# Performance work log

Hardware: AMD Instinct MI355X
Metric: run time of the kernel (lower is better)

The kernel has to match this reference:

```python
import jax, jax.numpy as jnp
import numpy as np

D_MODEL = 1024
MAX_LEN = 2048
BATCH = 4


def _causal_mask(max_len):
    # tril ones -> 0 on/below diag, -inf above (added to scores BEFORE scaling,
    # matching the original module's order of operations)
    return jnp.where(jnp.tril(jnp.ones((max_len, max_len), dtype=bool)), 0.0, -jnp.inf).astype(jnp.float32)


def setup_inputs() -> dict:
    key = jax.random.key(0)
    ks = jax.random.split(key, 9)
    s = 1.0 / np.sqrt(D_MODEL)  # torch Linear default init scale (uniform bound)
    return {
        "encoded_q": jax.random.normal(ks[0], (BATCH, MAX_LEN, D_MODEL), jnp.float32),
        "encoded_k": jax.random.normal(ks[1], (BATCH, MAX_LEN, D_MODEL), jnp.float32),
        "encoded_v": jax.random.normal(ks[2], (BATCH, MAX_LEN, D_MODEL), jnp.float32),
        "W_q": jax.random.uniform(ks[3], (D_MODEL, D_MODEL), jnp.float32, -s, s),
        "b_q": jax.random.uniform(ks[4], (D_MODEL,), jnp.float32, -s, s),
        "W_k": jax.random.uniform(ks[5], (D_MODEL, D_MODEL), jnp.float32, -s, s),
        "b_k": jax.random.uniform(ks[6], (D_MODEL,), jnp.float32, -s, s),
        "W_v": jax.random.uniform(ks[7], (D_MODEL, D_MODEL), jnp.float32, -s, s),
        "b_v": jax.random.uniform(ks[8], (D_MODEL,), jnp.float32, -s, s),
        "parameter_mask": 1,
    }


def reference(encoded_q, encoded_k, encoded_v, W_q, b_q, W_k, b_k, W_v, b_v, parameter_mask):
    # torch Linear: y = x @ W.T + b
    q = jnp.einsum("bsd,ed->bse", encoded_q, W_q) + b_q  # [B,S,D]
    k = jnp.einsum("bsd,ed->bse", encoded_k, W_k) + b_k
    v = jnp.einsum("bsd,ed->bse", encoded_v, W_v) + b_v
    values = jnp.einsum("bqd,bkd->bqk", q, k)  # [B,S,S]
    if parameter_mask:
        values = values + _causal_mask(values.shape[-1])
    scaled = values / jnp.sqrt(jnp.float32(D_MODEL))
    attn = jax.nn.softmax(scaled, axis=-1)
    return jnp.einsum("bqk,bkd->bqd", attn, v)  # [B,S,D]
```

## Files before the change

### kernel.cpp

```cpp
#include <hip/hip_runtime.h>

typedef __bf16 bf16;
typedef __attribute__((ext_vector_type(8))) __bf16 bf16x8;
typedef __attribute__((ext_vector_type(4))) __bf16 bf16x4;
typedef __attribute__((ext_vector_type(4))) float f32x4;

#define S_LEN 2048
#define DM 1024
#define NB 4

__device__ __forceinline__ void async_copy16(const void* g, void* l)
{
    __builtin_amdgcn_global_load_lds(
        (const __attribute__((address_space(1))) unsigned int*)g,
        (__attribute__((address_space(3))) unsigned int*)l,
        16, 0, 0);
}

#define VM_WAIT8 asm volatile("s_waitcnt vmcnt(8)" ::: "memory")
#define VM_WAIT0 asm volatile("s_waitcnt vmcnt(0)" ::: "memory")
#define LGKM0    asm volatile("s_waitcnt lgkmcnt(0)" ::: "memory")
#define BAR      asm volatile("s_barrier" ::: "memory")


__device__ __forceinline__ void stage_issue(const char* aGk, size_t aRow32,
                                            const char* bGk, size_t bRow32,
                                            char* aL, char* bL)
{
#pragma unroll
    for (int i = 0; i < 4; i++) {
        async_copy16(aGk + i * aRow32, aL + i * 4096);
        async_copy16(bGk + i * bRow32, bL + i * 4096);
    }
}

__device__ __forceinline__ void read_frags(const char* bufA, const char* bufB,
                                           int wr, int wc, int l16, int quad,
                                           bf16x8 (&af)[2][4], bf16x8 (&bfr)[2][4])
{
    const int swz = l16 & 7;
#pragma unroll
    for (int kk = 0; kk < 2; kk++) {
        const int col = (((kk << 2) + quad) ^ swz) << 4;
#pragma unroll
        for (int t = 0; t < 4; t++) {
            af[kk][t]  = *(const bf16x8*)(bufA + (wr * 64 + t * 16 + l16) * 128 + col);
            bfr[kk][t] = *(const bf16x8*)(bufB + (wc * 64 + t * 16 + l16) * 128 + col);
        }
    }
}

__device__ __forceinline__ void mfma_all(const bf16x8 (&af)[2][4],
                                         const bf16x8 (&bfr)[2][4],
                                         f32x4 (&acc)[4][4])
{
#pragma unroll
    for (int kk = 0; kk < 2; kk++)
#pragma unroll
        for (int rt = 0; rt < 4; rt++)
#pragma unroll
            for (int ct = 0; ct < 4; ct++)
                acc[rt][ct] = __builtin_amdgcn_mfma_f32_16x16x32_bf16(
                    af[kk][rt], bfr[kk][ct], acc[rt][ct], 0, 0, 0);
}

__device__ __forceinline__ void gemm_tile(
    const bf16* __restrict__ A, int lda,
    const bf16* __restrict__ B, int ldb,
    int kSteps, char* smem, f32x4 (&acc)[4][4])
{
    const int tid = threadIdx.x;
    const int w = tid >> 6, lane = tid & 63;
    const int quad = lane >> 4, l16 = lane & 15;
    const int wr = w >> 1, wc = w & 1;

#pragma unroll
    for (int i = 0; i < 4; i++)
#pragma unroll
        for (int j = 0; j < 4; j++) acc[i][j] = f32x4{0.f, 0.f, 0.f, 0.f};

    const int srow = tid >> 3;
    const int sc8  = tid & 7;
    const int srcCol = (sc8 ^ (srow & 7)) * 16;
    const char* aG = (const char*)(A + (size_t)srow * lda) + srcCol;
    const char* bG = (const char*)(B + (size_t)srow * ldb) + srcCol;
    const size_t aRow32 = (size_t)lda * 64;
    const size_t bRow32 = (size_t)ldb * 64;
    char* aL0 = smem +     0 + w * 1024;
    char* bL0 = smem + 16384 + w * 1024;
    char* aL1 = smem + 32768 + w * 1024;
    char* bL1 = smem + 49152 + w * 1024;

    stage_issue(aG,       aRow32, bG,       bRow32, aL0, bL0);
    stage_issue(aG + 128, aRow32, bG + 128, bRow32, aL1, bL1);

    for (int ks = 0; ks < kSteps; ks += 2) {
        const bool more = (ks + 2 < kSteps);
        bf16x8 af[2][4], bfr[2][4];

        VM_WAIT8;
        BAR;
        read_frags(smem, smem + 16384, wr, wc, l16, quad, af, bfr);
        LGKM0;
        BAR;
        if (more)
            stage_issue(aG + (size_t)(ks + 2) * 128, aRow32,
                        bG + (size_t)(ks + 2) * 128, bRow32, aL0, bL0);
        mfma_all(af, bfr, acc);

        if (more) { VM_WAIT8; } else { VM_WAIT0; }
        BAR;
        read_frags(smem + 32768, smem + 49152, wr, wc, l16, quad, af, bfr);
        LGKM0;
        BAR;
        if (more)
            stage_issue(aG + (size_t)(ks + 3) * 128, aRow32,
                        bG + (size_t)(ks + 3) * 128, bRow32, aL1, bL1);
        mfma_all(af, bfr, acc);
    }
}

__global__ __launch_bounds__(256) void cvt3_kernel(
    const float* __restrict__ s0, const float* __restrict__ s1, const float* __restrict__ s2,
    bf16* __restrict__ d0, bf16* __restrict__ d1, bf16* __restrict__ d2)
{
    const float* src = blockIdx.y == 0 ? s0 : blockIdx.y == 1 ? s1 : s2;
    bf16* dst        = blockIdx.y == 0 ? d0 : blockIdx.y == 1 ? d1 : d2;
    size_t i = ((size_t)blockIdx.x * 256 + threadIdx.x) * 8;
    f32x4 a = *(const f32x4*)(src + i);
    f32x4 b = *(const f32x4*)(src + i + 4);
    bf16x8 o;
    o[0] = (bf16)a[0]; o[1] = (bf16)a[1]; o[2] = (bf16)a[2]; o[3] = (bf16)a[3];
    o[4] = (bf16)b[0]; o[5] = (bf16)b[1]; o[6] = (bf16)b[2]; o[7] = (bf16)b[3];
    *(bf16x8*)(dst + i) = o;
}

__global__ __launch_bounds__(256) void proj_kernel(
    const bf16* __restrict__ Eq, const bf16* __restrict__ Ek, const bf16* __restrict__ Ev,
    const bf16* __restrict__ Wq, const bf16* __restrict__ Wk, const bf16* __restrict__ Wv,
    const float* __restrict__ bq, const float* __restrict__ bk, const float* __restrict__ bv,
    bf16* __restrict__ Qo, bf16* __restrict__ Ko, bf16* __restrict__ Vt)
{
    __shared__ __align__(16) char smem[65536];
    const int bid = blockIdx.x;
    const int c = bid & 7;
    const int j = bid >> 3;
    const int z = j >> 6;
    const int r64 = j & 63;
    const int m0 = (c * 8 + (r64 >> 3)) * 128;
    const int n0 = (r64 & 7) * 128;

    const bf16* E     = z == 0 ? Eq : z == 1 ? Ek : Ev;
    const bf16* W     = z == 0 ? Wq : z == 1 ? Wk : Wv;
    const float* bias = z == 0 ? bq : z == 1 ? bk : bv;

    f32x4 acc[4][4];
    gemm_tile(E + (size_t)m0 * DM, DM, W + (size_t)n0 * DM, DM, DM / 64, smem, acc);

    const int tid = threadIdx.x;
    const int w = tid >> 6, lane = tid & 63;
    const int quad = lane >> 4, l16 = lane & 15;
    const int wr = w >> 1, wc = w & 1;
    const int nBase = n0 + wc * 64;

    float bcol[4];
#pragma unroll
    for (int ct = 0; ct < 4; ct++) bcol[ct] = bias[nBase + ct * 16 + l16];

    __syncthreads();
    if (z < 2) {
        bf16* Tt = (bf16*)smem;
#pragma unroll
        for (int rt = 0; rt < 4; rt++)
#pragma unroll
            for (int ct = 0; ct < 4; ct++)
#pragma unroll
                for (int r = 0; r < 4; r++)
                    Tt[(wr * 64 + rt * 16 + quad * 4 + r) * 136 + wc * 64 + ct * 16 + l16]
                        = (bf16)(acc[rt][ct][r] + bcol[ct]);
        __syncthreads();
        bf16* O = z == 0 ? Qo : Ko;
        const int row = tid >> 1, half = tid & 1;
        const bf16* src = Tt + row * 136 + half * 64;
        bf16* dst = O + (size_t)(m0 + row) * DM + n0 + half * 64;
#pragma unroll
        for (int i = 0; i < 8; i++)
            *(bf16x8*)(dst + i * 8) = *(const bf16x8*)(src + i * 8);
    } else {
        const int mBase = m0 + wr * 64;
#pragma unroll
        for (int rt = 0; rt < 4; rt++) {
            const int m = mBase + rt * 16 + quad * 4;
            const int bb = m >> 11;
            const int s  = m & 2047;
#pragma unroll
            for (int ct = 0; ct < 4; ct++) {
                const int n = nBase + ct * 16 + l16;
                bf16x4 o;
                o[0] = (bf16)(acc[rt][ct][0] + bcol[ct]);
                o[1] = (bf16)(acc[rt][ct][1] + bcol[ct]);
                o[2] = (bf16)(acc[rt][ct][2] + bcol[ct]);
                o[3] = (bf16)(acc[rt][ct][3] + bcol[ct]);
                *(bf16x4*)(Vt + ((size_t)(bb * DM + n)) * S_LEN + s) = o;
            }
        }
    }
}

__global__ __launch_bounds__(256) void qk_kernel(
    const bf16* __restrict__ Q, const bf16* __restrict__ K,
    const int* __restrict__ maskp, bf16* __restrict__ P, float* __restrict__ lsum)
{
    const int bid = blockIdx.x;
    const int c = bid & 7;
    const int j = bid >> 3;
    const int b = j >> 5;
    const int jj = j & 31;
    const int kt = (jj < 16) ? c : (15 - c);
    const int qt = jj & 15;
    const bool causal = (maskp[0] != 0);
    if (causal && kt > qt) return;

    __shared__ __align__(16) char smem[65536];

    f32x4 acc[4][4];
    const bf16* Qb = Q + ((size_t)(b * S_LEN + qt * 128)) * DM;
    const bf16* Kb = K + ((size_t)(b * S_LEN + kt * 128)) * DM;
    gemm_tile(Qb, DM, Kb, DM, DM / 64, smem, acc);

    const int tid = threadIdx.x;
    const int w = tid >> 6, lane = tid & 63;
    const int quad = lane >> 4, l16 = lane & 15;
    const int wr = w >> 1, wc = w & 1;
    const float scale = 0.03125f;

    __syncthreads();
    bf16* Pt = (bf16*)smem;
#pragma unroll
    for (int rt = 0; rt < 4; rt++)
#pragma unroll
        for (int r = 0; r < 4; r++) {
            const int rloc = wr * 64 + rt * 16 + quad * 4 + r;
            const int qg = qt * 128 + rloc;
#pragma unroll
            for (int ct = 0; ct < 4; ct++) {
                const int kg = kt * 128 + wc * 64 + ct * 16 + l16;
                float p = (!causal || kg <= qg) ? __expf(acc[rt][ct][r] * scale) : 0.0f;
                Pt[rloc * 136 + wc * 64 + ct * 16 + l16] = (bf16)p;
            }
        }
    __syncthreads();

    bf16* Pb = P + (size_t)b * S_LEN * S_LEN;
    float* lb = lsum + b * S_LEN;
    const int row = tid >> 1, half = tid & 1;
    const bf16* src = Pt + row * 136 + half * 64;
    bf16* dst = Pb + (size_t)(qt * 128 + row) * S_LEN + kt * 128 + half * 64;
    float rs = 0.0f;
#pragma unroll
    for (int i = 0; i < 8; i++) {
        bf16x8 x = *(const bf16x8*)(src + i * 8);
        *(bf16x8*)(dst + i * 8) = x;
#pragma unroll
        for (int e = 0; e < 8; e++) rs += (float)x[e];
    }
    rs += __shfl_xor(rs, 1);
    if (half == 0) atomicAdd(&lb[qt * 128 + row], rs);
}

__global__ __launch_bounds__(256) void pv_kernel(
    const bf16* __restrict__ P, const bf16* __restrict__ Vt,
    const float* __restrict__ lsum, const int* __restrict__ maskp,
    float* __restrict__ Out)
{
    const int bid = blockIdx.x;
    const int dt = bid & 7;
    const int j = bid >> 3;
    const int b = j >> 4;
    const int qt = 15 - (j & 15);
    const bool causal = (maskp[0] != 0);
    const int kSteps = causal ? (qt + 1) * 2 : (S_LEN / 64);

    __shared__ __align__(16) char smem[65536];

    f32x4 acc[4][4];
    const bf16* Pb = P + ((size_t)b * S_LEN + qt * 128) * S_LEN;
    const bf16* Vb = Vt + ((size_t)(b * DM + dt * 128)) * S_LEN;
    gemm_tile(Pb, S_LEN, Vb, S_LEN, kSteps, smem, acc);

    const int tid = threadIdx.x;
    const int w = tid >> 6, lane = tid & 63;
    const int quad = lane >> 4, l16 = lane & 15;
    const int wr = w >> 1, wc = w & 1;

    const float* lb = lsum + b * S_LEN;
    float inv[4][4];
#pragma unroll
    for (int rt = 0; rt < 4; rt++)
#pragma unroll
        for (int r = 0; r < 4; r++)
            inv[rt][r] = 1.0f / lb[qt * 128 + wr * 64 + rt * 16 + quad * 4 + r];

    __syncthreads();
    float* Ot = (float*)smem;
#pragma unroll
    for (int h = 0; h < 2; h++) {
        if (wr == h) {
#pragma unroll
            for (int rt = 0; rt < 4; rt++)
#pragma unroll
                for (int r = 0; r < 4; r++) {
                    const int rloc = rt * 16 + quad * 4 + r;
#pragma unroll
                    for (int ct = 0; ct < 4; ct++)
                        Ot[rloc * 132 + wc * 64 + ct * 16 + l16] = acc[rt][ct][r] * inv[rt][r];
                }
        }
        __syncthreads();
        const int row = tid >> 2, qq = tid & 3;
        const float* src = Ot + row * 132 + qq * 32;
        float* dst = Out + (size_t)(b * S_LEN + qt * 128 + h * 64 + row) * DM + dt * 128 + qq * 32;
#pragma unroll
        for (int i = 0; i < 8; i++)
            *(f32x4*)(dst + i * 4) = *(const f32x4*)(src + i * 4);
        __syncthreads();
    }
}

extern "C" void kernel_launch(void* const* d_in, const int* in_sizes, int n_in,
                              void* d_out, int out_size, void* d_ws, size_t ws_size,
                              hipStream_t stream)
{
    const float* Eq = (const float*)d_in[0];
    const float* Ek = (const float*)d_in[1];
    const float* Ev = (const float*)d_in[2];
    const float* Wq = (const float*)d_in[3];
    const float* bq = (const float*)d_in[4];
    const float* Wk = (const float*)d_in[5];
    const float* bk = (const float*)d_in[6];
    const float* Wv = (const float*)d_in[7];
    const float* bv = (const float*)d_in[8];
    const int* maskp = (const int*)d_in[9];
    float* Out = (float*)d_out;

    char* ws = (char*)d_ws;
    const size_t SZ_QKV = (size_t)NB * S_LEN * DM * 2;
    const size_t SZ_W   = (size_t)DM * DM * 2;
    bf16* Qb  = (bf16*)(ws);
    bf16* Kb  = (bf16*)(ws + SZ_QKV);
    bf16* Vtb = (bf16*)(ws + 2 * SZ_QKV);
    bf16* Wqb = (bf16*)(ws + 3 * SZ_QKV);
    bf16* Wkb = (bf16*)(ws + 3 * SZ_QKV + SZ_W);
    bf16* Wvb = (bf16*)(ws + 3 * SZ_QKV + 2 * SZ_W);
    float* lsum = (float*)(ws + 3 * SZ_QKV + 3 * SZ_W);
    bf16* Pbuf = (bf16*)(ws + 3 * SZ_QKV + 3 * SZ_W + (1 << 20));
    bf16* Eqb = Pbuf;
    bf16* Ekb = Eqb + (size_t)NB * S_LEN * DM;
    bf16* Evb = Ekb + (size_t)NB * S_LEN * DM;

    hipMemsetAsync(lsum, 0, (size_t)NB * S_LEN * 4, stream);
    cvt3_kernel<<<dim3(512, 3), 256, 0, stream>>>(Wq, Wk, Wv, Wqb, Wkb, Wvb);
    cvt3_kernel<<<dim3(4096, 3), 256, 0, stream>>>(Eq, Ek, Ev, Eqb, Ekb, Evb);

    proj_kernel<<<1536, 256, 0, stream>>>(
        Eqb, Ekb, Evb, Wqb, Wkb, Wvb, bq, bk, bv, Qb, Kb, Vtb);

    qk_kernel<<<1024, 256, 0, stream>>>(Qb, Kb, maskp, Pbuf, lsum);
    pv_kernel<<<512, 256, 0, stream>>>(Pbuf, Vtb, lsum, maskp, Out);
}
```

Measured before the change: 297.6 us.

## Use 256x256 eight-wave pipelined GEMM tiles for projection and QK kernels

Adds a new 256x256 output-tile GEMM that runs eight waves and uses 128KB of LDS. It splits the MFMA work into quarter phases, interleaves async global-to-LDS staging between them, and raises MFMA priority with s_setprio. The projection and QK-score kernels move to this tile, with epilogues rewritten to write through LDS in two 128-row halves; causal QK enumerates only the lower-triangular tile pairs. The goal is more operand reuse per loaded byte and better overlap of loads with MFMA. In exchange the grids are much smaller: 144 causal QK blocks and 384 projection blocks, with likely one block per CU given the LDS size. That may underfill the GPU or leave tail waves.

```diff
diff --git a/kernel.cpp b/kernel.cpp
--- a/kernel.cpp
+++ b/kernel.cpp
@@ -19,8 +19,135 @@
 
 #define VM_WAIT8 asm volatile("s_waitcnt vmcnt(8)" ::: "memory")
 #define VM_WAIT0 asm volatile("s_waitcnt vmcnt(0)" ::: "memory")
+#define VM_WAIT(n) asm volatile("s_waitcnt vmcnt(" #n ")" ::: "memory")
 #define LGKM0    asm volatile("s_waitcnt lgkmcnt(0)" ::: "memory")
 #define BAR      asm volatile("s_barrier" ::: "memory")
+#define SCHED0   __builtin_amdgcn_sched_barrier(0)
+
+
+__device__ __forceinline__ void read_half_A(const char* base, int wr, int mh,
+                                            int l16, int quad, int swz,
+                                            bf16x8 (&af)[4][2])
+{
+#pragma unroll
+    for (int t = 0; t < 4; t++) {
+        const char* rp = base + (wr * 128 + mh * 64 + t * 16 + l16) * 128;
+        af[t][0] = *(const bf16x8*)(rp + ((quad ^ swz) << 4));
+        af[t][1] = *(const bf16x8*)(rp + (((4 + quad) ^ swz) << 4));
+    }
+}
+
+__device__ __forceinline__ void read_half_B(const char* base, int wc, int nh,
+                                            int l16, int quad, int swz,
+                                            bf16x8 (&bfr)[4][2])
+{
+#pragma unroll
+    for (int u = 0; u < 2; u++) {
+        const char* rp = base + (wc * 64 + nh * 32 + u * 16 + l16) * 128;
+        bfr[nh * 2 + u][0] = *(const bf16x8*)(rp + ((quad ^ swz) << 4));
+        bfr[nh * 2 + u][1] = *(const bf16x8*)(rp + (((4 + quad) ^ swz) << 4));
+    }
+}
+
+#define MFMA_Q(MH, NH) do {                                                   \
+    __builtin_amdgcn_s_setprio(1);                                            \
+    _Pragma("unroll")                                                         \
+    for (int kk = 0; kk < 2; kk++)                                            \
+    _Pragma("unroll")                                                         \
+    for (int mt = 0; mt < 4; mt++)                                            \
+    _Pragma("unroll")                                                         \
+    for (int nn = 0; nn < 2; nn++)                                            \
+        acc[(MH)*4 + mt][(NH)*2 + nn] = __builtin_amdgcn_mfma_f32_16x16x32_bf16( \
+            af[mt][kk], bfr[(NH)*2 + nn][kk], acc[(MH)*4 + mt][(NH)*2 + nn], 0, 0, 0); \
+    __builtin_amdgcn_s_setprio(0);                                            \
+} while (0)
+
+#define STAGE(Xg, ld2, ktt, h, lbase) do {                                    \
+    const char* _g = (Xg) + (size_t)(ktt) * 128 + (size_t)(h) * 128 * (ld2);  \
+    async_copy16(_g,             (lbase) + (h) * 16384);                      \
+    async_copy16(_g + 64 * (ld2), (lbase) + (h) * 16384 + 8192);              \
+} while (0)
+
+__device__ __forceinline__ void gemm256(
+    const bf16* __restrict__ A, int lda,
+    const bf16* __restrict__ B, int ldb,
+    int nt, char* smem, f32x4 (&acc)[8][4])
+{
+    const int tid = threadIdx.x;
+    const int w = tid >> 6, lane = tid & 63;
+    const int quad = lane >> 4, l16 = lane & 15;
+    const int wr = w >> 2, wc = w & 3;
+    const int swz = l16 & 7;
+
+#pragma unroll
+    for (int i = 0; i < 8; i++)
+#pragma unroll
+        for (int j = 0; j < 4; j++) acc[i][j] = f32x4{0.f, 0.f, 0.f, 0.f};
+
+    const size_t lda2 = (size_t)lda * 2, ldb2 = (size_t)ldb * 2;
+    const int srow = tid >> 3;
+    const int scol = ((tid & 7) ^ (srow & 7)) << 4;
+    const char* aG = (const char*)A + (size_t)srow * lda2 + scol;
+    const char* bG = (const char*)B + (size_t)srow * ldb2 + scol;
+    char* const lsw = smem + w * 1024;
+
+    bf16x8 af[4][2], bfr[4][2];
+
+    STAGE(bG, ldb2, 0, 0, lsw + 32768);
+    STAGE(bG, ldb2, 0, 1, lsw + 32768);
+    STAGE(aG, lda2, 0, 0, lsw);
+    STAGE(aG, lda2, 0, 1, lsw);
+    STAGE(bG, ldb2, 1, 0, lsw + 98304);
+    VM_WAIT(4); BAR;
+
+    for (int kt = 0; kt < nt; kt += 2) {
+        const int k1 = kt + 1;
+        const int k2 = (kt + 2 < nt) ? kt + 2 : kt;
+        const int k3 = (kt + 3 < nt) ? kt + 3 : kt;
+
+        read_half_A(smem,          wr, 0, l16, quad, swz, af);
+        read_half_B(smem + 32768,  wc, 0, l16, quad, swz, bfr);
+        STAGE(bG, ldb2, k1, 1, lsw + 98304);
+        BAR; LGKM0; SCHED0;
+        MFMA_Q(0, 0);
+        BAR;
+        read_half_B(smem + 32768,  wc, 1, l16, quad, swz, bfr);
+        STAGE(aG, lda2, k1, 0, lsw + 65536);
+        BAR; LGKM0; SCHED0;
+        MFMA_Q(0, 1);
+        VM_WAIT(6); BAR;
+        read_half_A(smem,          wr, 1, l16, quad, swz, af);
+        STAGE(aG, lda2, k1, 1, lsw + 65536);
+        BAR; LGKM0; SCHED0;
+        MFMA_Q(1, 1);
+        BAR;
+        STAGE(bG, ldb2, k2, 0, lsw + 32768);
+        BAR;
+        MFMA_Q(1, 0);
+        VM_WAIT(4); BAR;
+        read_half_A(smem + 65536,  wr, 0, l16, quad, swz, af);
+        read_half_B(smem + 98304,  wc, 0, l16, quad, swz, bfr);
+        STAGE(bG, ldb2, k2, 1, lsw + 32768);
+        BAR; LGKM0; SCHED0;
+        MFMA_Q(0, 0);
+        BAR;
+        read_half_B(smem + 98304,  wc, 1, l16, quad, swz, bfr);
+        STAGE(aG, lda2, k2, 0, lsw);
+        BAR; LGKM0; SCHED0;
+        MFMA_Q(0, 1);
+        VM_WAIT(6); BAR;
+        read_half_A(smem + 65536,  wr, 1, l16, quad, swz, af);
+        STAGE(aG, lda2, k2, 1, lsw);
+        BAR; LGKM0; SCHED0;
+        MFMA_Q(1, 1);
+        BAR;
+        STAGE(bG, ldb2, k3, 0, lsw + 98304);
+        BAR;
+        MFMA_Q(1, 0);
+        VM_WAIT(4); BAR;
+    }
+    VM_WAIT0; BAR;
+}
 
 
 __device__ __forceinline__ void stage_issue(const char* aGk, size_t aRow32,
@@ -135,62 +262,67 @@
     *(bf16x8*)(dst + i) = o;
 }
 
-__global__ __launch_bounds__(256) void proj_kernel(
+__global__ __launch_bounds__(512, 2) void proj_kernel(
     const bf16* __restrict__ Eq, const bf16* __restrict__ Ek, const bf16* __restrict__ Ev,
     const bf16* __restrict__ Wq, const bf16* __restrict__ Wk, const bf16* __restrict__ Wv,
     const float* __restrict__ bq, const float* __restrict__ bk, const float* __restrict__ bv,
     bf16* __restrict__ Qo, bf16* __restrict__ Ko, bf16* __restrict__ Vt)
 {
-    __shared__ __align__(16) char smem[65536];
+    __shared__ __align__(16) char smem[131072];
     const int bid = blockIdx.x;
     const int c = bid & 7;
     const int j = bid >> 3;
-    const int z = j >> 6;
-    const int r64 = j & 63;
-    const int m0 = (c * 8 + (r64 >> 3)) * 128;
-    const int n0 = (r64 & 7) * 128;
+    const int z = j >> 4;
+    const int jj = j & 15;
+    const int T = c * 16 + jj;
+    const int m0 = (T >> 2) * 256;
+    const int n0 = (T & 3) * 256;
 
     const bf16* E     = z == 0 ? Eq : z == 1 ? Ek : Ev;
     const bf16* W     = z == 0 ? Wq : z == 1 ? Wk : Wv;
     const float* bias = z == 0 ? bq : z == 1 ? bk : bv;
 
-    f32x4 acc[4][4];
-    gemm_tile(E + (size_t)m0 * DM, DM, W + (size_t)n0 * DM, DM, DM / 64, smem, acc);
+    f32x4 acc[8][4];
+    gemm256(E + (size_t)m0 * DM, DM, W + (size_t)n0 * DM, DM, DM / 64, smem, acc);
 
     const int tid = threadIdx.x;
     const int w = tid >> 6, lane = tid & 63;
     const int quad = lane >> 4, l16 = lane & 15;
-    const int wr = w >> 1, wc = w & 1;
+    const int wr = w >> 2, wc = w & 3;
     const int nBase = n0 + wc * 64;
 
     float bcol[4];
 #pragma unroll
     for (int ct = 0; ct < 4; ct++) bcol[ct] = bias[nBase + ct * 16 + l16];
 
-    __syncthreads();
     if (z < 2) {
         bf16* Tt = (bf16*)smem;
-#pragma unroll
-        for (int rt = 0; rt < 4; rt++)
-#pragma unroll
-            for (int ct = 0; ct < 4; ct++)
-#pragma unroll
-                for (int r = 0; r < 4; r++)
-                    Tt[(wr * 64 + rt * 16 + quad * 4 + r) * 136 + wc * 64 + ct * 16 + l16]
-                        = (bf16)(acc[rt][ct][r] + bcol[ct]);
-        __syncthreads();
         bf16* O = z == 0 ? Qo : Ko;
-        const int row = tid >> 1, half = tid & 1;
-        const bf16* src = Tt + row * 136 + half * 64;
-        bf16* dst = O + (size_t)(m0 + row) * DM + n0 + half * 64;
-#pragma unroll
-        for (int i = 0; i < 8; i++)
-            *(bf16x8*)(dst + i * 8) = *(const bf16x8*)(src + i * 8);
+#pragma unroll
+        for (int h = 0; h < 2; h++) {
+            if (wr == h) {
+#pragma unroll
+                for (int rt = 0; rt < 8; rt++)
+#pragma unroll
+                    for (int ct = 0; ct < 4; ct++)
+#pragma unroll
+                        for (int r = 0; r < 4; r++)
+                            Tt[(rt * 16 + quad * 4 + r) * 264 + wc * 64 + ct * 16 + l16]
+                                = (bf16)(acc[rt][ct][r] + bcol[ct]);
+            }
+            __syncthreads();
+            const int row = tid >> 2, seg = tid & 3;
+            const bf16* src = Tt + row * 264 + seg * 64;
+            bf16* dst = O + (size_t)(m0 + h * 128 + row) * DM + n0 + seg * 64;
+#pragma unroll
+            for (int i = 0; i < 8; i++)
+                *(bf16x8*)(dst + i * 8) = *(const bf16x8*)(src + i * 8);
+            __syncthreads();
+        }
     } else {
-        const int mBase = m0 + wr * 64;
-#pragma unroll
-        for (int rt = 0; rt < 4; rt++) {
-            const int m = mBase + rt * 16 + quad * 4;
+#pragma unroll
+        for (int rt = 0; rt < 8; rt++) {
+            const int m = m0 + wr * 128 + rt * 16 + quad * 4;
             const int bb = m >> 11;
             const int s  = m & 2047;
 #pragma unroll
@@ -207,65 +339,77 @@
     }
 }
 
-__global__ __launch_bounds__(256) void qk_kernel(
+__global__ __launch_bounds__(512, 2) void qk_kernel(
     const bf16* __restrict__ Q, const bf16* __restrict__ K,
     const int* __restrict__ maskp, bf16* __restrict__ P, float* __restrict__ lsum)
 {
     const int bid = blockIdx.x;
-    const int c = bid & 7;
-    const int j = bid >> 3;
-    const int b = j >> 5;
-    const int jj = j & 31;
-    const int kt = (jj < 16) ? c : (15 - c);
-    const int qt = jj & 15;
     const bool causal = (maskp[0] != 0);
-    if (causal && kt > qt) return;
-
-    __shared__ __align__(16) char smem[65536];
-
-    f32x4 acc[4][4];
-    const bf16* Qb = Q + ((size_t)(b * S_LEN + qt * 128)) * DM;
-    const bf16* Kb = K + ((size_t)(b * S_LEN + kt * 128)) * DM;
-    gemm_tile(Qb, DM, Kb, DM, DM / 64, smem, acc);
+    int b, qt, kt;
+    if (causal) {
+        if (bid >= 144) return;
+        b = bid / 36;
+        const int r = bid % 36;
+        qt = 0;
+        while ((qt + 1) * (qt + 2) / 2 <= r) qt++;
+        kt = r - qt * (qt + 1) / 2;
+    } else {
+        b = bid >> 6;
+        const int r = bid & 63;
+        qt = r >> 3; kt = r & 7;
+    }
+
+    __shared__ __align__(16) char smem[131072];
+
+    f32x4 acc[8][4];
+    gemm256(Q + ((size_t)(b * S_LEN) + qt * 256) * DM, DM,
+            K + ((size_t)(b * S_LEN) + kt * 256) * DM, DM, DM / 64, smem, acc);
 
     const int tid = threadIdx.x;
     const int w = tid >> 6, lane = tid & 63;
     const int quad = lane >> 4, l16 = lane & 15;
-    const int wr = w >> 1, wc = w & 1;
+    const int wr = w >> 2, wc = w & 3;
     const float scale = 0.03125f;
 
-    __syncthreads();
-    bf16* Pt = (bf16*)smem;
-#pragma unroll
-    for (int rt = 0; rt < 4; rt++)
-#pragma unroll
-        for (int r = 0; r < 4; r++) {
-            const int rloc = wr * 64 + rt * 16 + quad * 4 + r;
-            const int qg = qt * 128 + rloc;
-#pragma unroll
-            for (int ct = 0; ct < 4; ct++) {
-                const int kg = kt * 128 + wc * 64 + ct * 16 + l16;
-                float p = (!causal || kg <= qg) ? __expf(acc[rt][ct][r] * scale) : 0.0f;
-                Pt[rloc * 136 + wc * 64 + ct * 16 + l16] = (bf16)p;
-            }
-        }
-    __syncthreads();
-
+    bf16* Tt = (bf16*)smem;
     bf16* Pb = P + (size_t)b * S_LEN * S_LEN;
     float* lb = lsum + b * S_LEN;
-    const int row = tid >> 1, half = tid & 1;
-    const bf16* src = Pt + row * 136 + half * 64;
-    bf16* dst = Pb + (size_t)(qt * 128 + row) * S_LEN + kt * 128 + half * 64;
-    float rs = 0.0f;
-#pragma unroll
-    for (int i = 0; i < 8; i++) {
-        bf16x8 x = *(const bf16x8*)(src + i * 8);
-        *(bf16x8*)(dst + i * 8) = x;
-#pragma unroll
-        for (int e = 0; e < 8; e++) rs += (float)x[e];
-    }
-    rs += __shfl_xor(rs, 1);
-    if (half == 0) atomicAdd(&lb[qt * 128 + row], rs);
+
+#pragma unroll
+    for (int h = 0; h < 2; h++) {
+        if (wr == h) {
+#pragma unroll
+            for (int rt = 0; rt < 8; rt++)
+#pragma unroll
+                for (int r = 0; r < 4; r++) {
+                    const int rloc = rt * 16 + quad * 4 + r;
+                    const int qg = qt * 256 + h * 128 + rloc;
+#pragma unroll
+                    for (int ct = 0; ct < 4; ct++) {
+                        const int kg = kt * 256 + wc * 64 + ct * 16 + l16;
+                        const float p = (!causal || kg <= qg)
+                                            ? __expf(acc[rt][ct][r] * scale) : 0.0f;
+                        Tt[rloc * 264 + wc * 64 + ct * 16 + l16] = (bf16)p;
+                    }
+                }
+        }
+        __syncthreads();
+        const int row = tid >> 2, seg = tid & 3;
+        const bf16* src = Tt + row * 264 + seg * 64;
+        bf16* dst = Pb + (size_t)(qt * 256 + h * 128 + row) * S_LEN + kt * 256 + seg * 64;
+        float rs = 0.0f;
+#pragma unroll
+        for (int i = 0; i < 8; i++) {
+            bf16x8 x = *(const bf16x8*)(src + i * 8);
+            *(bf16x8*)(dst + i * 8) = x;
+#pragma unroll
+            for (int e = 0; e < 8; e++) rs += (float)x[e];
+        }
+        rs += __shfl_xor(rs, 1);
+        rs += __shfl_xor(rs, 2);
+        if ((tid & 3) == 0) atomicAdd(&lb[qt * 256 + h * 128 + row], rs);
+        __syncthreads();
+    }
 }
 
 __global__ __launch_bounds__(256) void pv_kernel(
@@ -362,9 +506,9 @@
     cvt3_kernel<<<dim3(512, 3), 256, 0, stream>>>(Wq, Wk, Wv, Wqb, Wkb, Wvb);
     cvt3_kernel<<<dim3(4096, 3), 256, 0, stream>>>(Eq, Ek, Ev, Eqb, Ekb, Evb);
 
-    proj_kernel<<<1536, 256, 0, stream>>>(
+    proj_kernel<<<384, 512, 0, stream>>>(
         Eqb, Ekb, Evb, Wqb, Wkb, Wvb, bq, bk, bv, Qb, Kb, Vtb);
 
-    qk_kernel<<<1024, 256, 0, stream>>>(Qb, Kb, maskp, Pbuf, lsum);
+    qk_kernel<<<256, 512, 0, stream>>>(Qb, Kb, maskp, Pbuf, lsum);
     pv_kernel<<<512, 256, 0, stream>>>(Pbuf, Vtb, lsum, maskp, Out);
 }
```

Result: slower. 310.7 us (+4.4%).

## Co-schedule V projection with QK^T scores kernel and remap PV block order

Applied to the files above, without the earlier changes.

Splits the projection kernel so Q and K are computed first, then launches a combined kernel whose first 512 blocks compute the V projection while the remaining blocks compute the causal QK^T exp tiles. This fills the GPU with mixed work, so the V projection can overlap the lightly loaded, causally skipped score tiles instead of running as a separate launch. It also changes the PV block index mapping to interleave batches and query-tile parity, aiming for better load balance across XCDs. The combined kernel may raise register pressure because of its two code paths.

```diff
diff --git a/kernel.cpp b/kernel.cpp
--- a/kernel.cpp
+++ b/kernel.cpp
@@ -135,11 +135,11 @@
     *(bf16x8*)(dst + i) = o;
 }
 
-__global__ __launch_bounds__(256) void proj_kernel(
-    const bf16* __restrict__ Eq, const bf16* __restrict__ Ek, const bf16* __restrict__ Ev,
-    const bf16* __restrict__ Wq, const bf16* __restrict__ Wk, const bf16* __restrict__ Wv,
-    const float* __restrict__ bq, const float* __restrict__ bk, const float* __restrict__ bv,
-    bf16* __restrict__ Qo, bf16* __restrict__ Ko, bf16* __restrict__ Vt)
+__global__ __launch_bounds__(256) void projqk_kernel(
+    const bf16* __restrict__ Eq, const bf16* __restrict__ Ek,
+    const bf16* __restrict__ Wq, const bf16* __restrict__ Wk,
+    const float* __restrict__ bq, const float* __restrict__ bk,
+    bf16* __restrict__ Qo, bf16* __restrict__ Ko)
 {
     __shared__ __align__(16) char smem[65536];
     const int bid = blockIdx.x;
@@ -150,9 +150,9 @@
     const int m0 = (c * 8 + (r64 >> 3)) * 128;
     const int n0 = (r64 & 7) * 128;
 
-    const bf16* E     = z == 0 ? Eq : z == 1 ? Ek : Ev;
-    const bf16* W     = z == 0 ? Wq : z == 1 ? Wk : Wv;
-    const float* bias = z == 0 ? bq : z == 1 ? bk : bv;
+    const bf16* E     = z == 0 ? Eq : Ek;
+    const bf16* W     = z == 0 ? Wq : Wk;
+    const float* bias = z == 0 ? bq : bk;
 
     f32x4 acc[4][4];
     gemm_tile(E + (size_t)m0 * DM, DM, W + (size_t)n0 * DM, DM, DM / 64, smem, acc);
@@ -168,25 +168,52 @@
     for (int ct = 0; ct < 4; ct++) bcol[ct] = bias[nBase + ct * 16 + l16];
 
     __syncthreads();
-    if (z < 2) {
-        bf16* Tt = (bf16*)smem;
-#pragma unroll
-        for (int rt = 0; rt < 4; rt++)
-#pragma unroll
-            for (int ct = 0; ct < 4; ct++)
-#pragma unroll
-                for (int r = 0; r < 4; r++)
-                    Tt[(wr * 64 + rt * 16 + quad * 4 + r) * 136 + wc * 64 + ct * 16 + l16]
-                        = (bf16)(acc[rt][ct][r] + bcol[ct]);
-        __syncthreads();
-        bf16* O = z == 0 ? Qo : Ko;
-        const int row = tid >> 1, half = tid & 1;
-        const bf16* src = Tt + row * 136 + half * 64;
-        bf16* dst = O + (size_t)(m0 + row) * DM + n0 + half * 64;
-#pragma unroll
-        for (int i = 0; i < 8; i++)
-            *(bf16x8*)(dst + i * 8) = *(const bf16x8*)(src + i * 8);
-    } else {
+    bf16* Tt = (bf16*)smem;
+#pragma unroll
+    for (int rt = 0; rt < 4; rt++)
+#pragma unroll
+        for (int ct = 0; ct < 4; ct++)
+#pragma unroll
+            for (int r = 0; r < 4; r++)
+                Tt[(wr * 64 + rt * 16 + quad * 4 + r) * 136 + wc * 64 + ct * 16 + l16]
+                    = (bf16)(acc[rt][ct][r] + bcol[ct]);
+    __syncthreads();
+    bf16* O = z == 0 ? Qo : Ko;
+    const int row = tid >> 1, half = tid & 1;
+    const bf16* src = Tt + row * 136 + half * 64;
+    bf16* dst = O + (size_t)(m0 + row) * DM + n0 + half * 64;
+#pragma unroll
+    for (int i = 0; i < 8; i++)
+        *(bf16x8*)(dst + i * 8) = *(const bf16x8*)(src + i * 8);
+}
+
+__global__ __launch_bounds__(256) void projv_qk_kernel(
+    const bf16* __restrict__ Ev, const bf16* __restrict__ Wv,
+    const float* __restrict__ bv, bf16* __restrict__ Vt,
+    const bf16* __restrict__ Q, const bf16* __restrict__ K,
+    const int* __restrict__ maskp, bf16* __restrict__ P, float* __restrict__ lsum)
+{
+    __shared__ __align__(16) char smem[65536];
+    const int bid = blockIdx.x;
+    const int tid = threadIdx.x;
+    const int w = tid >> 6, lane = tid & 63;
+    const int quad = lane >> 4, l16 = lane & 15;
+    const int wr = w >> 1, wc = w & 1;
+
+    if (bid < 512) {
+        const int c = bid & 7;
+        const int r64 = bid >> 3;
+        const int m0 = (c * 8 + (r64 >> 3)) * 128;
+        const int n0 = (r64 & 7) * 128;
+
+        f32x4 acc[4][4];
+        gemm_tile(Ev + (size_t)m0 * DM, DM, Wv + (size_t)n0 * DM, DM, DM / 64, smem, acc);
+
+        const int nBase = n0 + wc * 64;
+        float bcol[4];
+#pragma unroll
+        for (int ct = 0; ct < 4; ct++) bcol[ct] = bv[nBase + ct * 16 + l16];
+
         const int mBase = m0 + wr * 64;
 #pragma unroll
         for (int rt = 0; rt < 4; rt++) {
@@ -204,68 +231,57 @@
                 *(bf16x4*)(Vt + ((size_t)(bb * DM + n)) * S_LEN + s) = o;
             }
         }
-    }
-}
-
-__global__ __launch_bounds__(256) void qk_kernel(
-    const bf16* __restrict__ Q, const bf16* __restrict__ K,
-    const int* __restrict__ maskp, bf16* __restrict__ P, float* __restrict__ lsum)
-{
-    const int bid = blockIdx.x;
-    const int c = bid & 7;
-    const int j = bid >> 3;
-    const int b = j >> 5;
-    const int jj = j & 31;
-    const int kt = (jj < 16) ? c : (15 - c);
-    const int qt = jj & 15;
-    const bool causal = (maskp[0] != 0);
-    if (causal && kt > qt) return;
-
-    __shared__ __align__(16) char smem[65536];
-
-    f32x4 acc[4][4];
-    const bf16* Qb = Q + ((size_t)(b * S_LEN + qt * 128)) * DM;
-    const bf16* Kb = K + ((size_t)(b * S_LEN + kt * 128)) * DM;
-    gemm_tile(Qb, DM, Kb, DM, DM / 64, smem, acc);
-
-    const int tid = threadIdx.x;
-    const int w = tid >> 6, lane = tid & 63;
-    const int quad = lane >> 4, l16 = lane & 15;
-    const int wr = w >> 1, wc = w & 1;
-    const float scale = 0.03125f;
-
-    __syncthreads();
-    bf16* Pt = (bf16*)smem;
-#pragma unroll
-    for (int rt = 0; rt < 4; rt++)
-#pragma unroll
-        for (int r = 0; r < 4; r++) {
-            const int rloc = wr * 64 + rt * 16 + quad * 4 + r;
-            const int qg = qt * 128 + rloc;
-#pragma unroll
-            for (int ct = 0; ct < 4; ct++) {
-                const int kg = kt * 128 + wc * 64 + ct * 16 + l16;
-                float p = (!causal || kg <= qg) ? __expf(acc[rt][ct][r] * scale) : 0.0f;
-                Pt[rloc * 136 + wc * 64 + ct * 16 + l16] = (bf16)p;
+    } else {
+        const int qbid = bid - 512;
+        const int c = qbid & 7;
+        const int j = qbid >> 3;
+        const int b = j >> 5;
+        const int jj = j & 31;
+        const int kt = (jj < 16) ? c : (15 - c);
+        const int qt = jj & 15;
+        const bool causal = (maskp[0] != 0);
+        if (causal && kt > qt) return;
+
+        f32x4 acc[4][4];
+        const bf16* Qb = Q + ((size_t)(b * S_LEN + qt * 128)) * DM;
+        const bf16* Kb = K + ((size_t)(b * S_LEN + kt * 128)) * DM;
+        gemm_tile(Qb, DM, Kb, DM, DM / 64, smem, acc);
+
+        const float scale = 0.03125f;
+
+        __syncthreads();
+        bf16* Pt = (bf16*)smem;
+#pragma unroll
+        for (int rt = 0; rt < 4; rt++)
+#pragma unroll
+            for (int r = 0; r < 4; r++) {
+                const int rloc = wr * 64 + rt * 16 + quad * 4 + r;
+                const int qg = qt * 128 + rloc;
+#pragma unroll
+                for (int ct = 0; ct < 4; ct++) {
+                    const int kg = kt * 128 + wc * 64 + ct * 16 + l16;
+                    float p = (!causal || kg <= qg) ? __expf(acc[rt][ct][r] * scale) : 0.0f;
+                    Pt[rloc * 136 + wc * 64 + ct * 16 + l16] = (bf16)p;
+                }
             }
+        __syncthreads();
+
+        bf16* Pb = P + (size_t)b * S_LEN * S_LEN;
+        float* lb = lsum + b * S_LEN;
+        const int row = tid >> 1, half = tid & 1;
+        const bf16* src = Pt + row * 136 + half * 64;
+        bf16* dst = Pb + (size_t)(qt * 128 + row) * S_LEN + kt * 128 + half * 64;
+        float rs = 0.0f;
+#pragma unroll
+        for (int i = 0; i < 8; i++) {
+            bf16x8 x = *(const bf16x8*)(src + i * 8);
+            *(bf16x8*)(dst + i * 8) = x;
+#pragma unroll
+            for (int e = 0; e < 8; e++) rs += (float)x[e];
         }
-    __syncthreads();
-
-    bf16* Pb = P + (size_t)b * S_LEN * S_LEN;
-    float* lb = lsum + b * S_LEN;
-    const int row = tid >> 1, half = tid & 1;
-    const bf16* src = Pt + row * 136 + half * 64;
-    bf16* dst = Pb + (size_t)(qt * 128 + row) * S_LEN + kt * 128 + half * 64;
-    float rs = 0.0f;
-#pragma unroll
-    for (int i = 0; i < 8; i++) {
-        bf16x8 x = *(const bf16x8*)(src + i * 8);
-        *(bf16x8*)(dst + i * 8) = x;
-#pragma unroll
-        for (int e = 0; e < 8; e++) rs += (float)x[e];
-    }
-    rs += __shfl_xor(rs, 1);
-    if (half == 0) atomicAdd(&lb[qt * 128 + row], rs);
+        rs += __shfl_xor(rs, 1);
+        if (half == 0) atomicAdd(&lb[qt * 128 + row], rs);
+    }
 }
 
 __global__ __launch_bounds__(256) void pv_kernel(
@@ -274,10 +290,13 @@
     float* __restrict__ Out)
 {
     const int bid = blockIdx.x;
-    const int dt = bid & 7;
-    const int j = bid >> 3;
-    const int b = j >> 4;
-    const int qt = 15 - (j & 15);
+    const int c = bid & 7;
+    const int b = c >> 1;
+    const int par = c & 1;
+    const int idx = bid >> 3;
+    const int dt = idx & 7;
+    const int qi = idx >> 3;
+    const int qt = (7 - qi) * 2 + par;
     const bool causal = (maskp[0] != 0);
     const int kSteps = causal ? (qt + 1) * 2 : (S_LEN / 64);
 
@@ -362,9 +381,11 @@
     cvt3_kernel<<<dim3(512, 3), 256, 0, stream>>>(Wq, Wk, Wv, Wqb, Wkb, Wvb);
     cvt3_kernel<<<dim3(4096, 3), 256, 0, stream>>>(Eq, Ek, Ev, Eqb, Ekb, Evb);
 
-    proj_kernel<<<1536, 256, 0, stream>>>(
-        Eqb, Ekb, Evb, Wqb, Wkb, Wvb, bq, bk, bv, Qb, Kb, Vtb);
-
-    qk_kernel<<<1024, 256, 0, stream>>>(Qb, Kb, maskp, Pbuf, lsum);
+    projqk_kernel<<<1024, 256, 0, stream>>>(
+        Eqb, Ekb, Wqb, Wkb, bq, bk, Qb, Kb);
+
+    projv_qk_kernel<<<1536, 256, 0, stream>>>(
+        Evb, Wvb, bv, Vtb, Qb, Kb, maskp, Pbuf, lsum);
+
     pv_kernel<<<512, 256, 0, stream>>>(Pbuf, Vtb, lsum, maskp, Out);
 }
```

Result: faster. 280.9 us (-5.6%).
